# Kernel optimization log

Hardware: AMD Instinct MI355X
Metric: run time of the kernel (lower is better)

The kernel has to match this reference:

```python
import jax, jax.numpy as jnp
import numpy as np

N, E = 50000, 800000
H, KC, EC, NH = 64, 64, 32, 4   # hidden, key, edge channels, heads
HPH, KPH = H // NH, KC // NH    # per-head value/key dims (16, 16)


def ssp(x):
    # ShiftedSoftplus
    return jax.nn.softplus(x) - jnp.log(2.0).astype(x.dtype)


def grouped_lin(x, w):
    # x: (N, NH, in_per_head), w: (NH, out_per_head, in_per_head)
    # equivalent to Conv1d(kernel=1, groups=NH, bias=False)
    return jnp.einsum('nhi,hoi->nho', x, w)


def lin(x, w, b):
    return x @ w.T + b


def segment_softmax(logits, seg, num_segments):
    # logits: (E, NH), seg: (E,)
    m = jax.ops.segment_max(logits, seg, num_segments=num_segments)
    m = jnp.where(jnp.isfinite(m), m, 0.0)
    e = jnp.exp(logits - m[seg])
    s = jax.ops.segment_sum(e, seg, num_segments=num_segments)
    return e / s[seg]


def setup_inputs() -> dict:
    key = jax.random.key(0)
    ks = jax.random.split(key, 24)
    sc = 0.05
    inp = {
        'x': jax.random.normal(ks[0], (N, H), jnp.float32),
        'edge_index': jax.random.randint(ks[1], (2, E), 0, N, jnp.int64),
        'edge_attr': jax.random.normal(ks[2], (E, EC), jnp.float32),
        # grouped 1x1 convs (block-diagonal linears), no bias
        'k_w': jax.random.normal(ks[3], (NH, KPH, HPH), jnp.float32) * sc,
        'q_w': jax.random.normal(ks[4], (NH, KPH, HPH), jnp.float32) * sc,
        'v_w': jax.random.normal(ks[5], (NH, HPH, HPH), jnp.float32) * sc,
        # weight_k_net: Linear(EC,KPH) -> ssp -> Linear(KPH,KPH)
        'wkn_w1': jax.random.normal(ks[6], (KPH, EC), jnp.float32) * sc,
        'wkn_b1': jnp.zeros((KPH,), jnp.float32),
        'wkn_w2': jax.random.normal(ks[7], (KPH, KPH), jnp.float32) * sc,
        'wkn_b2': jnp.zeros((KPH,), jnp.float32),
        'wkl_w': jax.random.normal(ks[8], (KPH, KPH), jnp.float32) * sc,
        'wkl_b': jnp.zeros((KPH,), jnp.float32),
        # weight_v_net: Linear(EC,HPH) -> ssp -> Linear(HPH,HPH)
        'wvn_w1': jax.random.normal(ks[9], (HPH, EC), jnp.float32) * sc,
        'wvn_b1': jnp.zeros((HPH,), jnp.float32),
        'wvn_w2': jax.random.normal(ks[10], (HPH, HPH), jnp.float32) * sc,
        'wvn_b2': jnp.zeros((HPH,), jnp.float32),
        'wvl_w': jax.random.normal(ks[11], (HPH, HPH), jnp.float32) * sc,
        'wvl_b': jnp.zeros((HPH,), jnp.float32),
        'cen_w': jax.random.normal(ks[12], (H, H), jnp.float32) * sc,
        'cen_b': jnp.zeros((H,), jnp.float32),
        'out_w': jax.random.normal(ks[13], (H, H), jnp.float32) * sc,
        'out_b': jnp.zeros((H,), jnp.float32),
    }
    return inp


def reference(x, edge_index, edge_attr, k_w, q_w, v_w,
              wkn_w1, wkn_b1, wkn_w2, wkn_b2, wkl_w, wkl_b,
              wvn_w1, wvn_b1, wvn_w2, wvn_b2, wvl_w, wvl_b,
              cen_w, cen_b, out_w, out_b):
    n = x.shape[0]
    row, col = edge_index[0], edge_index[1]
    xh = x.reshape(n, NH, HPH)                       # per-head split of channels
    h_keys = grouped_lin(xh, k_w)                    # (N, NH, KPH)
    h_queries = grouped_lin(xh, q_w)                 # (N, NH, KPH)
    h_values = grouped_lin(xh, v_w)                  # (N, NH, HPH)

    W_k = lin(ssp(lin(edge_attr, wkn_w1, wkn_b1)), wkn_w2, wkn_b2)   # (E, KPH)
    keys_j = lin(W_k[:, None, :] * h_keys[col], wkl_w, wkl_b)        # (E, NH, KPH)
    queries_i = h_queries[row]                                       # (E, NH, KPH)
    qk_ij = jnp.sum(queries_i * keys_j, axis=-1)                     # (E, NH)
    alpha = segment_softmax(qk_ij, row, n)                           # (E, NH)

    W_v = lin(ssp(lin(edge_attr, wvn_w1, wvn_b1)), wvn_w2, wvn_b2)   # (E, HPH)
    msg_j = lin(W_v[:, None, :] * h_values[col], wvl_w, wvl_b)       # (E, NH, HPH)
    msg_j = alpha[:, :, None] * msg_j
    aggr = jax.ops.segment_sum(msg_j, row, num_segments=n).reshape(n, H)

    out = lin(x, cen_w, cen_b) + aggr
    return lin(ssp(out), out_w, out_b)
```

## Files before the change

### kernel.cpp

```cpp
#include <hip/hip_runtime.h>
#include <math.h>
#include <stdint.h>

#define NN 50000
#define NE 800000
#define HD 64
#define ECH 32
#define NHEAD 4
#define NBLK 196
#define NEBLK (NE / 256)

static_assert(NE % 256 == 0, "edge kernel assumes full blocks");

typedef __attribute__((ext_vector_type(8))) short bf8;
typedef __attribute__((ext_vector_type(4))) float f32x4;
typedef __attribute__((ext_vector_type(2))) float v2f;
typedef __attribute__((ext_vector_type(2))) __bf16 v2bf;

#define LOG2E 1.44269504088896340736f
#define LN2   0.69314718055994530942f

__device__ __forceinline__ float ssp_f(float v) {
    float t = __builtin_amdgcn_exp2f(-fabsf(v) * LOG2E);
    return fmaxf(v, 0.0f) + LN2 * __builtin_amdgcn_logf(1.0f + t) - LN2;
}
__device__ __forceinline__ float bf2f(uint32_t b) { return __uint_as_float(b << 16); }

__device__ __forceinline__ uint32_t cvt_pk_bf16(float lo, float hi) {
    v2f v = {lo, hi};
    v2bf b = __builtin_convertvector(v, v2bf);
    return __builtin_bit_cast(uint32_t, b);
}
__device__ __forceinline__ v2f bfpair(uint32_t p) {
    v2f r;
    r.x = __uint_as_float(p << 16);
    r.y = __uint_as_float(p & 0xffff0000u);
    return r;
}
__device__ __forceinline__ uint4 pack8c(const float* s) {
    uint4 r;
    r.x = cvt_pk_bf16(s[0], s[1]);
    r.y = cvt_pk_bf16(s[2], s[3]);
    r.z = cvt_pk_bf16(s[4], s[5]);
    r.w = cvt_pk_bf16(s[6], s[7]);
    return r;
}
__device__ __forceinline__ bf8 pack_bf8(float4 a, float4 b) {
    union { uint32_t u[4]; bf8 v; } r;
    r.u[0] = cvt_pk_bf16(a.x, a.y);
    r.u[1] = cvt_pk_bf16(a.z, a.w);
    r.u[2] = cvt_pk_bf16(b.x, b.y);
    r.u[3] = cvt_pk_bf16(b.z, b.w);
    return r.v;
}
__device__ __forceinline__ bf8 zero_bf8() {
    bf8 r;
    #pragma unroll
    for (int i = 0; i < 8; ++i) r[i] = 0;
    return r;
}

__global__ __launch_bounds__(256) void node_count_kernel(
    const float* __restrict__ x, const int* __restrict__ ei,
    const float* __restrict__ k_w, const float* __restrict__ q_w, const float* __restrict__ v_w,
    const float* __restrict__ wkl_w, const float* __restrict__ wkl_b,
    uint16_t* __restrict__ qtq, uint16_t* __restrict__ hkv,
    int* __restrict__ counts)
{
    atomicAdd(counts + ei[blockIdx.x * 256 + threadIdx.x], 1);

    if (blockIdx.x >= NBLK) return;
    __shared__ float skw[NHEAD * 256], sqw[NHEAD * 256], svw[NHEAD * 256];
    __shared__ float s_kl[256], s_klb[16];
    for (int i = threadIdx.x; i < NHEAD * 256; i += 256) {
        skw[i] = k_w[i]; sqw[i] = q_w[i]; svw[i] = v_w[i];
    }
    if (threadIdx.x < 256) s_kl[threadIdx.x] = wkl_w[threadIdx.x] * LOG2E;
    if (threadIdx.x < 16) s_klb[threadIdx.x] = wkl_b[threadIdx.x] * LOG2E;
    __syncthreads();
    int n = blockIdx.x * 256 + threadIdx.x;
    if (n >= NN) return;
    const float* xn = x + (size_t)n * HD;
    uint16_t* qrow = qtq + (size_t)n * 72;
    uint16_t* kvrow = hkv + (size_t)n * 128;
    float qbv[NHEAD];
    for (int h = 0; h < NHEAD; ++h) {
        v2f xr2[8];
        {
            const float4* xp = (const float4*)(xn + h * 16);
            #pragma unroll
            for (int j = 0; j < 4; ++j) {
                float4 t4 = xp[j];
                xr2[2 * j] = (v2f){t4.x, t4.y};
                xr2[2 * j + 1] = (v2f){t4.z, t4.w};
            }
        }
        float rq[16], rk[16], rv[16];
        for (int o = 0; o < 16; ++o) {
            const v2f* wq = (const v2f*)(sqw + h * 256 + o * 16);
            const v2f* wk = (const v2f*)(skw + h * 256 + o * 16);
            const v2f* wv = (const v2f*)(svw + h * 256 + o * 16);
            v2f sq = {0.f, 0.f}, sk = {0.f, 0.f}, sv = {0.f, 0.f};
            #pragma unroll
            for (int j = 0; j < 8; ++j) {
                sq += xr2[j] * wq[j];
                sk += xr2[j] * wk[j];
                sv += xr2[j] * wv[j];
            }
            rq[o] = sq.x + sq.y; rk[o] = sk.x + sk.y; rv[o] = sv.x + sv.y;
        }
        float rqt[16];
        #pragma unroll
        for (int ip = 0; ip < 8; ++ip) {
            v2f s2 = {0.f, 0.f};
            #pragma unroll
            for (int o = 0; o < 16; ++o) {
                v2f kl = *(const v2f*)(s_kl + o * 16 + 2 * ip);
                v2f q2 = {rq[o], rq[o]};
                s2 += q2 * kl;
            }
            rqt[2 * ip] = s2.x; rqt[2 * ip + 1] = s2.y;
        }
        float qbh = 0.f;
        #pragma unroll
        for (int o = 0; o < 16; ++o) qbh += rq[o] * s_klb[o];
        qbv[h] = qbh;

        uint4* oq = (uint4*)(qrow + h * 16);
        uint4* ok = (uint4*)(kvrow + h * 16);
        uint4* ov = (uint4*)(kvrow + 64 + h * 16);
        oq[0] = pack8c(rqt); oq[1] = pack8c(rqt + 8);
        ok[0] = pack8c(rk);  ok[1] = pack8c(rk + 8);
        ov[0] = pack8c(rv);  ov[1] = pack8c(rv + 8);
    }
    *(float4*)(qrow + 64) = *(float4*)&qbv[0];
}

__global__ __launch_bounds__(256) void scan_bsum_kernel(
    const int* __restrict__ counts, int* __restrict__ bsum)
{
    __shared__ int sd[256];
    int i = blockIdx.x * 256 + threadIdx.x;
    sd[threadIdx.x] = (i < NN) ? counts[i] : 0;
    __syncthreads();
    for (int s = 128; s > 0; s >>= 1) {
        if (threadIdx.x < (unsigned)s) sd[threadIdx.x] += sd[threadIdx.x + s];
        __syncthreads();
    }
    if (threadIdx.x == 0) bsum[blockIdx.x] = sd[0];
}

__global__ __launch_bounds__(256) void scan_top_kernel(int* __restrict__ bsum)
{
    __shared__ int tmp[256];
    int v = (threadIdx.x < NBLK) ? bsum[threadIdx.x] : 0;
    tmp[threadIdx.x] = v;
    __syncthreads();
    for (int d = 1; d < 256; d <<= 1) {
        int t = (threadIdx.x >= (unsigned)d) ? tmp[threadIdx.x - d] : 0;
        __syncthreads();
        tmp[threadIdx.x] += t;
        __syncthreads();
    }
    if (threadIdx.x < NBLK) bsum[threadIdx.x] = tmp[threadIdx.x] - v;
}

__global__ __launch_bounds__(256) void scan_final_kernel(
    const int* __restrict__ counts, const int* __restrict__ bsum,
    int* __restrict__ offsets, int* __restrict__ cursor)
{
    __shared__ int tmp[256];
    int i = blockIdx.x * 256 + threadIdx.x;
    int v = (i < NN) ? counts[i] : 0;
    tmp[threadIdx.x] = v;
    __syncthreads();
    for (int d = 1; d < 256; d <<= 1) {
        int t = (threadIdx.x >= (unsigned)d) ? tmp[threadIdx.x - d] : 0;
        __syncthreads();
        tmp[threadIdx.x] += t;
        __syncthreads();
    }
    int excl = tmp[threadIdx.x] - v + bsum[blockIdx.x];
    if (i < NN) { offsets[i] = excl; cursor[i] = excl; }
}

__global__ __launch_bounds__(256) void scatter_kernel(
    const int* __restrict__ ei, int* __restrict__ cursor,
    int* __restrict__ elist, uint32_t* __restrict__ rcp)
{
    int e = blockIdx.x * 256 + threadIdx.x;
    if (e >= NE) return;
    int r = ei[e];
    int c = ei[NE + e];
    int pos = atomicAdd(cursor + r, 1);
    elist[pos] = e;
    rcp[pos] = ((uint32_t)r << 16) | (uint32_t)c;
}

__global__ __launch_bounds__(256) void edge_compute_kernel(
    const int* __restrict__ elist, const uint32_t* __restrict__ rcp,
    const float* __restrict__ ea,
    const float* __restrict__ wkn_w1, const float* __restrict__ wkn_b1,
    const float* __restrict__ wkn_w2, const float* __restrict__ wkn_b2,
    const float* __restrict__ wvn_w1, const float* __restrict__ wvn_b1,
    const float* __restrict__ wvn_w2, const float* __restrict__ wvn_b2,
    const uint16_t* __restrict__ qtq, const uint16_t* __restrict__ hkv,
    uint16_t* __restrict__ payload, float* __restrict__ wfac)
{
    __shared__ uint16_t s_trA[4][64][24];
    __shared__ uint16_t s_trB[4][64][24];

    const int w = threadIdx.x >> 6;
    const int L = threadIdx.x & 63;
    const int m = L & 15;
    const int g = L >> 4;
    const int ebase = blockIdx.x * 256 + w * 64;

    int eidv[4];
    uint32_t rcv[4];
    #pragma unroll
    for (int t = 0; t < 4; ++t) eidv[t] = elist[ebase + 16 * t + m];
    #pragma unroll
    for (int t = 0; t < 4; ++t) rcv[t] = rcp[ebase + 16 * t + m];

    bf8 eaf[4];
    #pragma unroll
    for (int t = 0; t < 4; ++t) {
        const float* er = ea + (size_t)eidv[t] * ECH + 8 * g;
        eaf[t] = pack_bf8(*(const float4*)er, *(const float4*)(er + 4));
    }
    bf8 w1kf, w1vf, w2kf, w2vf;
    {
        const float* p = wkn_w1 + m * 32 + 8 * g;
        w1kf = pack_bf8(*(const float4*)p, *(const float4*)(p + 4));
        p = wvn_w1 + m * 32 + 8 * g;
        w1vf = pack_bf8(*(const float4*)p, *(const float4*)(p + 4));
        if (g < 2) {
            p = wkn_w2 + m * 16 + 8 * g;
            w2kf = pack_bf8(*(const float4*)p, *(const float4*)(p + 4));
            p = wvn_w2 + m * 16 + 8 * g;
            w2vf = pack_bf8(*(const float4*)p, *(const float4*)(p + 4));
        } else {
            w2kf = zero_bf8(); w2vf = zero_bf8();
        }
    }
    float4 b1k = *(const float4*)(wkn_b1 + 4 * g);
    float4 b1v = *(const float4*)(wvn_b1 + 4 * g);
    float4 b2k = *(const float4*)(wkn_b2 + 4 * g);
    float4 b2v = *(const float4*)(wvn_b2 + 4 * g);

    #pragma unroll
    for (int t = 0; t < 4; ++t) {
        f32x4 acc = {b1k.x, b1k.y, b1k.z, b1k.w};
        acc = __builtin_amdgcn_mfma_f32_16x16x32_bf16(w1kf, eaf[t], acc, 0, 0, 0);
        uint2 pk;
        pk.x = cvt_pk_bf16(ssp_f(acc[0]), ssp_f(acc[1]));
        pk.y = cvt_pk_bf16(ssp_f(acc[2]), ssp_f(acc[3]));
        *(uint2*)&s_trA[w][16 * t + m][4 * g] = pk;
    }
    bf8 l1k[4];
    #pragma unroll
    for (int t = 0; t < 4; ++t)
        l1k[t] = (g < 2) ? *(const bf8*)&s_trA[w][16 * t + m][8 * g] : zero_bf8();
    #pragma unroll
    for (int t = 0; t < 4; ++t) {
        f32x4 acc = {b1v.x, b1v.y, b1v.z, b1v.w};
        acc = __builtin_amdgcn_mfma_f32_16x16x32_bf16(w1vf, eaf[t], acc, 0, 0, 0);
        uint2 pk;
        pk.x = cvt_pk_bf16(ssp_f(acc[0]), ssp_f(acc[1]));
        pk.y = cvt_pk_bf16(ssp_f(acc[2]), ssp_f(acc[3]));
        *(uint2*)&s_trA[w][16 * t + m][4 * g] = pk;
    }
    bf8 l1v[4];
    #pragma unroll
    for (int t = 0; t < 4; ++t)
        l1v[t] = (g < 2) ? *(const bf8*)&s_trA[w][16 * t + m][8 * g] : zero_bf8();

    #pragma unroll
    for (int t = 0; t < 4; ++t) {
        f32x4 acc = {b2k.x, b2k.y, b2k.z, b2k.w};
        acc = __builtin_amdgcn_mfma_f32_16x16x32_bf16(w2kf, l1k[t], acc, 0, 0, 0);
        uint2 pk;
        pk.x = cvt_pk_bf16(acc[0], acc[1]);
        pk.y = cvt_pk_bf16(acc[2], acc[3]);
        *(uint2*)&s_trB[w][16 * t + m][4 * g] = pk;

        f32x4 accv = {b2v.x, b2v.y, b2v.z, b2v.w};
        accv = __builtin_amdgcn_mfma_f32_16x16x32_bf16(w2vf, l1v[t], accv, 0, 0, 0);
        uint2 pv;
        pv.x = cvt_pk_bf16(accv[0], accv[1]);
        pv.y = cvt_pk_bf16(accv[2], accv[3]);
        *(uint2*)&s_trA[w][16 * t + m][4 * g] = pv;
    }

    #pragma unroll
    for (int t = 0; t < 4; ++t) {
        const int E = ebase + 16 * t + m;
        const int row = (int)(rcv[t] >> 16), col = (int)(rcv[t] & 0xffffu);

        uint32_t wk_u[8], wv_u[8];
        *(uint4*)&wk_u[0] = *(const uint4*)&s_trB[w][16 * t + m][0];
        *(uint4*)&wk_u[4] = *(const uint4*)&s_trB[w][16 * t + m][8];
        *(uint4*)&wv_u[0] = *(const uint4*)&s_trA[w][16 * t + m][0];
        *(uint4*)&wv_u[4] = *(const uint4*)&s_trA[w][16 * t + m][8];

        const uint16_t* qrow = qtq + (size_t)row * 72;
        const uint16_t* kvrow = hkv + (size_t)col * 128;
        uint32_t q_u[8], k_u[8], v_u[8];
        *(uint4*)&q_u[0] = *(const uint4*)(qrow + 16 * g);
        *(uint4*)&q_u[4] = *(const uint4*)(qrow + 16 * g + 8);
        *(uint4*)&k_u[0] = *(const uint4*)(kvrow + 16 * g);
        *(uint4*)&k_u[4] = *(const uint4*)(kvrow + 16 * g + 8);
        *(uint4*)&v_u[0] = *(const uint4*)(kvrow + 64 + 16 * g);
        *(uint4*)&v_u[4] = *(const uint4*)(kvrow + 64 + 16 * g + 8);

        v2f qk2 = {0.f, 0.f};
        #pragma unroll
        for (int i = 0; i < 8; ++i)
            qk2 += bfpair(q_u[i]) * (bfpair(wk_u[i]) * bfpair(k_u[i]));
        float qk = *(const float*)(qrow + 64 + 2 * g) + qk2.x + qk2.y;
        float wgt = __builtin_amdgcn_exp2f(qk);
        v2f wgt2 = {wgt, wgt};

        uint32_t po[8];
        #pragma unroll
        for (int i = 0; i < 8; ++i) {
            v2f o2 = (bfpair(wv_u[i]) * bfpair(v_u[i])) * wgt2;
            po[i] = cvt_pk_bf16(o2.x, o2.y);
        }
        uint4* pd = (uint4*)(payload + (size_t)E * HD + 16 * g);
        pd[0] = *(uint4*)&po[0];
        pd[1] = *(uint4*)&po[4];
        wfac[(size_t)E * NHEAD + g] = wgt;
    }
}

__global__ __launch_bounds__(256) void gather_kernel(
    const uint16_t* __restrict__ payload, const float* __restrict__ wfac,
    const int* __restrict__ offsets, const int* __restrict__ counts,
    float* __restrict__ mout)
{
    const int n = (blockIdx.x * 256 + threadIdx.x) >> 6;
    if (n >= NN) return;
    const int L = threadIdx.x & 63;
    const int q = L & 7;
    const int g = L >> 3;
    const int h = q >> 1;

    const int st = offsets[n];
    const int deg = counts[n];

    v2f u2[4] = {{0.f,0.f},{0.f,0.f},{0.f,0.f},{0.f,0.f}};
    float ds = 0.f;
    const uint16_t* pp = payload + (size_t)st * HD + 8 * q;
    const float* wp = wfac + (size_t)st * NHEAD + h;
    const int iters = (deg + 7) >> 3;
    for (int i = 0; i < iters; i += 2) {
        const int e0 = 8 * i + g;
        const int e1 = e0 + 8;
        if (e0 < deg) {
            uint4 pv = *(const uint4*)(pp + (size_t)e0 * HD);
            u2[0] += bfpair(pv.x); u2[1] += bfpair(pv.y);
            u2[2] += bfpair(pv.z); u2[3] += bfpair(pv.w);
            ds += wp[(size_t)e0 * NHEAD];
        }
        if (e1 < deg) {
            uint4 pv = *(const uint4*)(pp + (size_t)e1 * HD);
            u2[0] += bfpair(pv.x); u2[1] += bfpair(pv.y);
            u2[2] += bfpair(pv.z); u2[3] += bfpair(pv.w);
            ds += wp[(size_t)e1 * NHEAD];
        }
    }
    #pragma unroll
    for (int s = 8; s < 64; s <<= 1) {
        #pragma unroll
        for (int j = 0; j < 4; ++j) {
            u2[j].x += __shfl_xor(u2[j].x, s);
            u2[j].y += __shfl_xor(u2[j].y, s);
        }
        ds += __shfl_xor(ds, s);
    }
    if (g == 0) {
        float inv = (deg > 0) ? (1.f / ds) : 0.f;
        float r0[4] = {u2[0].x * inv, u2[0].y * inv, u2[1].x * inv, u2[1].y * inv};
        float r1[4] = {u2[2].x * inv, u2[2].y * inv, u2[3].x * inv, u2[3].y * inv};
        float* mr = mout + (size_t)n * HD + 8 * q;
        *(float4*)mr = *(float4*)r0;
        *(float4*)(mr + 4) = *(float4*)r1;
    }
}

__global__ __launch_bounds__(256) void finalize_kernel(
    const float* __restrict__ x, const float* __restrict__ m,
    const int* __restrict__ counts,
    const float* __restrict__ wvl_w, const float* __restrict__ wvl_b,
    const float* __restrict__ cen_w, const float* __restrict__ cen_b,
    const float* __restrict__ out_w, const float* __restrict__ out_b,
    float* __restrict__ out)
{
    __shared__ float s_cw[4096], s_ow[4096];
    __shared__ float s_x[4][64], s_m[4][64], s_t[4][64];
    for (int idx = threadIdx.x; idx < 4096; idx += 256) {
        int o = idx & 63, i = idx >> 6;
        s_cw[i * 64 + o] = cen_w[o * 64 + i];
        s_ow[i * 64 + o] = out_w[o * 64 + i];
    }
    __syncthreads();

    const int l = threadIdx.x >> 6;
    const int c = threadIdx.x & 63;
    const int hh = c >> 4;

    float wvlr[16];
    #pragma unroll
    for (int i = 0; i < 16; ++i) wvlr[i] = wvl_w[(c & 15) * 16 + i];
    const float vlb = wvl_b[c & 15];
    const float cb = cen_b[c];
    const float ob = out_b[c];

    const int n0 = blockIdx.x * 64 + l * 16;
    for (int t = 0; t < 16; ++t) {
        const int n = n0 + t;
        const bool valid = n < NN;
        const int deg = valid ? counts[n] : 0;
        s_x[l][c] = valid ? x[(size_t)n * HD + c] : 0.f;
        s_m[l][c] = valid ? m[(size_t)n * HD + c] : 0.f;

        float aggr = 0.f;
        if (deg > 0) {
            float s = vlb;
            #pragma unroll
            for (int i = 0; i < 16; ++i) s += s_m[l][hh * 16 + i] * wvlr[i];
            aggr = s;
        }
        float sc = cb;
        #pragma unroll 8
        for (int i = 0; i < 64; ++i) sc += s_x[l][i] * s_cw[i * 64 + c];
        sc += aggr;
        s_t[l][c] = ssp_f(sc);
        float so = ob;
        #pragma unroll 8
        for (int i = 0; i < 64; ++i) so += s_t[l][i] * s_ow[i * 64 + c];
        if (valid) out[(size_t)n * HD + c] = so;
    }
}

extern "C" void kernel_launch(void* const* d_in, const int* in_sizes, int n_in,
                              void* d_out, int out_size, void* d_ws, size_t ws_size,
                              hipStream_t stream)
{
    const float* x      = (const float*)d_in[0];
    const int*   ei     = (const int*)d_in[1];
    const float* ea     = (const float*)d_in[2];
    const float* k_w    = (const float*)d_in[3];
    const float* q_w    = (const float*)d_in[4];
    const float* v_w    = (const float*)d_in[5];
    const float* wkn_w1 = (const float*)d_in[6];
    const float* wkn_b1 = (const float*)d_in[7];
    const float* wkn_w2 = (const float*)d_in[8];
    const float* wkn_b2 = (const float*)d_in[9];
    const float* wkl_w  = (const float*)d_in[10];
    const float* wkl_b  = (const float*)d_in[11];
    const float* wvn_w1 = (const float*)d_in[12];
    const float* wvn_b1 = (const float*)d_in[13];
    const float* wvn_w2 = (const float*)d_in[14];
    const float* wvn_b2 = (const float*)d_in[15];
    const float* wvl_w  = (const float*)d_in[16];
    const float* wvl_b  = (const float*)d_in[17];
    const float* cen_w  = (const float*)d_in[18];
    const float* cen_b  = (const float*)d_in[19];
    const float* out_w  = (const float*)d_in[20];
    const float* out_b  = (const float*)d_in[21];
    float* out = (float*)d_out;

    float* wfac  = (float*)d_ws;
    uint16_t* qtq = (uint16_t*)(wfac + (size_t)NE * NHEAD);
    uint16_t* hkv = qtq + (size_t)NN * 72;
    uint16_t* payload = hkv + (size_t)NN * 128;
    uint32_t* rcp = (uint32_t*)(payload + (size_t)NE * HD);
    int* elist   = (int*)(rcp + (size_t)NE);
    int* counts  = elist + NE;
    int* bsum    = counts + NN;
    int* offsets = bsum + 256;
    int* cursor  = offsets + NN;
    float* mbuf  = (float*)hkv;

    hipMemsetAsync(counts, 0, (size_t)NN * sizeof(int), stream);
    node_count_kernel<<<NEBLK, 256, 0, stream>>>(
        x, ei, k_w, q_w, v_w, wkl_w, wkl_b, qtq, hkv, counts);
    scan_bsum_kernel<<<NBLK, 256, 0, stream>>>(counts, bsum);
    scan_top_kernel<<<1, 256, 0, stream>>>(bsum);
    scan_final_kernel<<<NBLK, 256, 0, stream>>>(counts, bsum, offsets, cursor);
    scatter_kernel<<<NEBLK, 256, 0, stream>>>(ei, cursor, elist, rcp);
    edge_compute_kernel<<<NEBLK, 256, 0, stream>>>(
        elist, rcp, ea, wkn_w1, wkn_b1, wkn_w2, wkn_b2,
        wvn_w1, wvn_b1, wvn_w2, wvn_b2,
        qtq, hkv, payload, wfac);
    gather_kernel<<<(NN * 64) / 256, 256, 0, stream>>>(
        payload, wfac, offsets, counts, mbuf);
    finalize_kernel<<<(NN + 63) / 64, 256, 0, stream>>>(
        x, mbuf, counts, wvl_w, wvl_b, cen_w, cen_b, out_w, out_b, out);
}
```

Baseline: 450.1 us.

## Fuse gather into edge kernel via in-wave segmented scan and atomics

Removes the per-edge bf16 payload and weight buffers and the separate gather kernel. Each wave now runs a segmented inclusive scan over 16 row-sorted edges using shuffles, and the segment ends atomically add fp32 partial sums and softmax denominators into per-node buffers. The finalize kernel divides by the accumulated denominator. This avoids writing and re-reading about 100MB of payload. In exchange it adds shuffle work, many float atomics to global memory, and an extra memset, and summation order becomes nondeterministic.

Result: slower. 789.3 us (+75.4%).

```diff
diff --git a/kernel.cpp b/kernel.cpp
--- a/kernel.cpp
+++ b/kernel.cpp
@@ -205,7 +205,7 @@
     const float* __restrict__ wvn_w1, const float* __restrict__ wvn_b1,
     const float* __restrict__ wvn_w2, const float* __restrict__ wvn_b2,
     const uint16_t* __restrict__ qtq, const uint16_t* __restrict__ hkv,
-    uint16_t* __restrict__ payload, float* __restrict__ wfac)
+    float* __restrict__ mraw, float* __restrict__ dsb)
 {
     __shared__ uint16_t s_trA[4][64][24];
     __shared__ uint16_t s_trB[4][64][24];
@@ -295,7 +295,6 @@
 
     #pragma unroll
     for (int t = 0; t < 4; ++t) {
-        const int E = ebase + 16 * t + m;
         const int row = (int)(rcv[t] >> 16), col = (int)(rcv[t] & 0xffffu);
 
         uint32_t wk_u[8], wv_u[8];
@@ -322,77 +321,39 @@
         float wgt = __builtin_amdgcn_exp2f(qk);
         v2f wgt2 = {wgt, wgt};
 
-        uint32_t po[8];
+        float o[17];
         #pragma unroll
         for (int i = 0; i < 8; ++i) {
             v2f o2 = (bfpair(wv_u[i]) * bfpair(v_u[i])) * wgt2;
-            po[i] = cvt_pk_bf16(o2.x, o2.y);
-        }
-        uint4* pd = (uint4*)(payload + (size_t)E * HD + 16 * g);
-        pd[0] = *(uint4*)&po[0];
-        pd[1] = *(uint4*)&po[4];
-        wfac[(size_t)E * NHEAD + g] = wgt;
-    }
-}
-
-__global__ __launch_bounds__(256) void gather_kernel(
-    const uint16_t* __restrict__ payload, const float* __restrict__ wfac,
-    const int* __restrict__ offsets, const int* __restrict__ counts,
-    float* __restrict__ mout)
-{
-    const int n = (blockIdx.x * 256 + threadIdx.x) >> 6;
-    if (n >= NN) return;
-    const int L = threadIdx.x & 63;
-    const int q = L & 7;
-    const int g = L >> 3;
-    const int h = q >> 1;
-
-    const int st = offsets[n];
-    const int deg = counts[n];
-
-    v2f u2[4] = {{0.f,0.f},{0.f,0.f},{0.f,0.f},{0.f,0.f}};
-    float ds = 0.f;
-    const uint16_t* pp = payload + (size_t)st * HD + 8 * q;
-    const float* wp = wfac + (size_t)st * NHEAD + h;
-    const int iters = (deg + 7) >> 3;
-    for (int i = 0; i < iters; i += 2) {
-        const int e0 = 8 * i + g;
-        const int e1 = e0 + 8;
-        if (e0 < deg) {
-            uint4 pv = *(const uint4*)(pp + (size_t)e0 * HD);
-            u2[0] += bfpair(pv.x); u2[1] += bfpair(pv.y);
-            u2[2] += bfpair(pv.z); u2[3] += bfpair(pv.w);
-            ds += wp[(size_t)e0 * NHEAD];
-        }
-        if (e1 < deg) {
-            uint4 pv = *(const uint4*)(pp + (size_t)e1 * HD);
-            u2[0] += bfpair(pv.x); u2[1] += bfpair(pv.y);
-            u2[2] += bfpair(pv.z); u2[3] += bfpair(pv.w);
-            ds += wp[(size_t)e1 * NHEAD];
-        }
-    }
-    #pragma unroll
-    for (int s = 8; s < 64; s <<= 1) {
+            o[2 * i] = o2.x; o[2 * i + 1] = o2.y;
+        }
+        o[16] = wgt;
+
         #pragma unroll
-        for (int j = 0; j < 4; ++j) {
-            u2[j].x += __shfl_xor(u2[j].x, s);
-            u2[j].y += __shfl_xor(u2[j].y, s);
-        }
-        ds += __shfl_xor(ds, s);
-    }
-    if (g == 0) {
-        float inv = (deg > 0) ? (1.f / ds) : 0.f;
-        float r0[4] = {u2[0].x * inv, u2[0].y * inv, u2[1].x * inv, u2[1].y * inv};
-        float r1[4] = {u2[2].x * inv, u2[2].y * inv, u2[3].x * inv, u2[3].y * inv};
-        float* mr = mout + (size_t)n * HD + 8 * q;
-        *(float4*)mr = *(float4*)r0;
-        *(float4*)(mr + 4) = *(float4*)r1;
+        for (int d = 1; d < 16; d <<= 1) {
+            const int srcl = (L - d) & 63;
+            const int prow = __shfl(row, srcl);
+            const bool take = (m >= d) && (prow == row);
+            #pragma unroll
+            for (int i = 0; i < 17; ++i) {
+                float pv = __shfl(o[i], srcl);
+                o[i] += take ? pv : 0.0f;
+            }
+        }
+        const int nrow = __shfl(row, (L + 1) & 63);
+        const bool segend = (m == 15) || (nrow != row);
+        if (segend) {
+            float* mr = mraw + (size_t)row * HD + 16 * g;
+            #pragma unroll
+            for (int i = 0; i < 16; ++i) atomicAdd(mr + i, o[i]);
+            atomicAdd(dsb + (size_t)row * NHEAD + g, o[16]);
+        }
     }
 }
 
 __global__ __launch_bounds__(256) void finalize_kernel(
-    const float* __restrict__ x, const float* __restrict__ m,
-    const int* __restrict__ counts,
+    const float* __restrict__ x, const float* __restrict__ mraw,
+    const float* __restrict__ dsb, const int* __restrict__ counts,
     const float* __restrict__ wvl_w, const float* __restrict__ wvl_b,
     const float* __restrict__ cen_w, const float* __restrict__ cen_b,
     const float* __restrict__ out_w, const float* __restrict__ out_b,
@@ -424,7 +385,12 @@
         const bool valid = n < NN;
         const int deg = valid ? counts[n] : 0;
         s_x[l][c] = valid ? x[(size_t)n * HD + c] : 0.f;
-        s_m[l][c] = valid ? m[(size_t)n * HD + c] : 0.f;
+        float mv = 0.f;
+        if (deg > 0) {
+            float dsv = dsb[(size_t)n * NHEAD + hh];
+            mv = mraw[(size_t)n * HD + c] * (1.0f / dsv);
+        }
+        s_m[l][c] = mv;
 
         float aggr = 0.f;
         if (deg > 0) {
@@ -473,19 +439,19 @@
     const float* out_b  = (const float*)d_in[21];
     float* out = (float*)d_out;
 
-    float* wfac  = (float*)d_ws;
-    uint16_t* qtq = (uint16_t*)(wfac + (size_t)NE * NHEAD);
+    uint16_t* qtq = (uint16_t*)d_ws;
     uint16_t* hkv = qtq + (size_t)NN * 72;
-    uint16_t* payload = hkv + (size_t)NN * 128;
-    uint32_t* rcp = (uint32_t*)(payload + (size_t)NE * HD);
+    float* mraw  = (float*)(hkv + (size_t)NN * 128);
+    float* dsb   = mraw + (size_t)NN * HD;
+    uint32_t* rcp = (uint32_t*)(dsb + (size_t)NN * NHEAD);
     int* elist   = (int*)(rcp + (size_t)NE);
     int* counts  = elist + NE;
     int* bsum    = counts + NN;
     int* offsets = bsum + 256;
     int* cursor  = offsets + NN;
-    float* mbuf  = (float*)hkv;
 
     hipMemsetAsync(counts, 0, (size_t)NN * sizeof(int), stream);
+    hipMemsetAsync(mraw, 0, (size_t)NN * (HD + NHEAD) * sizeof(float), stream);
     node_count_kernel<<<NEBLK, 256, 0, stream>>>(
         x, ei, k_w, q_w, v_w, wkl_w, wkl_b, qtq, hkv, counts);
     scan_bsum_kernel<<<NBLK, 256, 0, stream>>>(counts, bsum);
@@ -495,9 +461,7 @@
     edge_compute_kernel<<<NEBLK, 256, 0, stream>>>(
         elist, rcp, ea, wkn_w1, wkn_b1, wkn_w2, wkn_b2,
         wvn_w1, wvn_b1, wvn_w2, wvn_b2,
-        qtq, hkv, payload, wfac);
-    gather_kernel<<<(NN * 64) / 256, 256, 0, stream>>>(
-        payload, wfac, offsets, counts, mbuf);
+        qtq, hkv, mraw, dsb);
     finalize_kernel<<<(NN + 63) / 64, 256, 0, stream>>>(
-        x, mbuf, counts, wvl_w, wvl_b, cen_w, cen_b, out_w, out_b, out);
-}
+        x, mraw, dsb, counts, wvl_w, wvl_b, cen_w, cen_b, out_w, out_b, out);
+}
```

## Record per-edge rank during counting and drop separate scatter kernel

Applied to the files above, without the earlier changes.

The counting atomic now returns each edge's rank within its destination row, and the edge kernel computes its CSR slot as offsets[row]+rank. This removes the scatter pass and the elist/rcp buffers. The edge kernel now reads edge_attr and edge_index in their original contiguous order and scatters its payload writes instead of gathering edge_attr reads. In exchange, rows and columns are read as full ints rather than a packed word, and the edge kernel does an extra indirect offsets lookup.

Measured after the change: 448.6 us. No clear change (-0.3%).

```diff
diff --git a/kernel.cpp b/kernel.cpp
--- a/kernel.cpp
+++ b/kernel.cpp
@@ -65,9 +65,13 @@
     const float* __restrict__ k_w, const float* __restrict__ q_w, const float* __restrict__ v_w,
     const float* __restrict__ wkl_w, const float* __restrict__ wkl_b,
     uint16_t* __restrict__ qtq, uint16_t* __restrict__ hkv,
-    int* __restrict__ counts)
-{
-    atomicAdd(counts + ei[blockIdx.x * 256 + threadIdx.x], 1);
+    int* __restrict__ counts, int* __restrict__ rank)
+{
+    {
+        int e = blockIdx.x * 256 + threadIdx.x;
+        int r = ei[e];
+        rank[e] = atomicAdd(counts + r, 1);
+    }
 
     if (blockIdx.x >= NBLK) return;
     __shared__ float skw[NHEAD * 256], sqw[NHEAD * 256], svw[NHEAD * 256];
@@ -167,7 +171,7 @@
 
 __global__ __launch_bounds__(256) void scan_final_kernel(
     const int* __restrict__ counts, const int* __restrict__ bsum,
-    int* __restrict__ offsets, int* __restrict__ cursor)
+    int* __restrict__ offsets)
 {
     __shared__ int tmp[256];
     int i = blockIdx.x * 256 + threadIdx.x;
@@ -181,24 +185,12 @@
         __syncthreads();
     }
     int excl = tmp[threadIdx.x] - v + bsum[blockIdx.x];
-    if (i < NN) { offsets[i] = excl; cursor[i] = excl; }
-}
-
-__global__ __launch_bounds__(256) void scatter_kernel(
-    const int* __restrict__ ei, int* __restrict__ cursor,
-    int* __restrict__ elist, uint32_t* __restrict__ rcp)
-{
-    int e = blockIdx.x * 256 + threadIdx.x;
-    if (e >= NE) return;
-    int r = ei[e];
-    int c = ei[NE + e];
-    int pos = atomicAdd(cursor + r, 1);
-    elist[pos] = e;
-    rcp[pos] = ((uint32_t)r << 16) | (uint32_t)c;
+    if (i < NN) offsets[i] = excl;
 }
 
 __global__ __launch_bounds__(256) void edge_compute_kernel(
-    const int* __restrict__ elist, const uint32_t* __restrict__ rcp,
+    const int* __restrict__ ei, const int* __restrict__ rank,
+    const int* __restrict__ offsets,
     const float* __restrict__ ea,
     const float* __restrict__ wkn_w1, const float* __restrict__ wkn_b1,
     const float* __restrict__ wkn_w2, const float* __restrict__ wkn_b2,
@@ -216,17 +208,23 @@
     const int g = L >> 4;
     const int ebase = blockIdx.x * 256 + w * 64;
 
-    int eidv[4];
-    uint32_t rcv[4];
-    #pragma unroll
-    for (int t = 0; t < 4; ++t) eidv[t] = elist[ebase + 16 * t + m];
-    #pragma unroll
-    for (int t = 0; t < 4; ++t) rcv[t] = rcp[ebase + 16 * t + m];
+    int rows[4], cols[4], posv[4];
+    #pragma unroll
+    for (int t = 0; t < 4; ++t) {
+        const int e = ebase + 16 * t + m;
+        rows[t] = ei[e];
+        cols[t] = ei[NE + e];
+    }
+    #pragma unroll
+    for (int t = 0; t < 4; ++t) {
+        const int e = ebase + 16 * t + m;
+        posv[t] = offsets[rows[t]] + rank[e];
+    }
 
     bf8 eaf[4];
     #pragma unroll
     for (int t = 0; t < 4; ++t) {
-        const float* er = ea + (size_t)eidv[t] * ECH + 8 * g;
+        const float* er = ea + (size_t)(ebase + 16 * t + m) * ECH + 8 * g;
         eaf[t] = pack_bf8(*(const float4*)er, *(const float4*)(er + 4));
     }
     bf8 w1kf, w1vf, w2kf, w2vf;
@@ -295,8 +293,7 @@
 
     #pragma unroll
     for (int t = 0; t < 4; ++t) {
-        const int E = ebase + 16 * t + m;
-        const int row = (int)(rcv[t] >> 16), col = (int)(rcv[t] & 0xffffu);
+        const int row = rows[t], col = cols[t];
 
         uint32_t wk_u[8], wv_u[8];
         *(uint4*)&wk_u[0] = *(const uint4*)&s_trB[w][16 * t + m][0];
@@ -328,10 +325,10 @@
             v2f o2 = (bfpair(wv_u[i]) * bfpair(v_u[i])) * wgt2;
             po[i] = cvt_pk_bf16(o2.x, o2.y);
         }
-        uint4* pd = (uint4*)(payload + (size_t)E * HD + 16 * g);
+        uint4* pd = (uint4*)(payload + (size_t)posv[t] * HD + 16 * g);
         pd[0] = *(uint4*)&po[0];
         pd[1] = *(uint4*)&po[4];
-        wfac[(size_t)E * NHEAD + g] = wgt;
+        wfac[(size_t)posv[t] * NHEAD + g] = wgt;
     }
 }
 
@@ -477,23 +474,20 @@
     uint16_t* qtq = (uint16_t*)(wfac + (size_t)NE * NHEAD);
     uint16_t* hkv = qtq + (size_t)NN * 72;
     uint16_t* payload = hkv + (size_t)NN * 128;
-    uint32_t* rcp = (uint32_t*)(payload + (size_t)NE * HD);
-    int* elist   = (int*)(rcp + (size_t)NE);
-    int* counts  = elist + NE;
+    int* rank    = (int*)(payload + (size_t)NE * HD);
+    int* counts  = rank + NE;
     int* bsum    = counts + NN;
     int* offsets = bsum + 256;
-    int* cursor  = offsets + NN;
     float* mbuf  = (float*)hkv;
 
     hipMemsetAsync(counts, 0, (size_t)NN * sizeof(int), stream);
     node_count_kernel<<<NEBLK, 256, 0, stream>>>(
-        x, ei, k_w, q_w, v_w, wkl_w, wkl_b, qtq, hkv, counts);
+        x, ei, k_w, q_w, v_w, wkl_w, wkl_b, qtq, hkv, counts, rank);
     scan_bsum_kernel<<<NBLK, 256, 0, stream>>>(counts, bsum);
     scan_top_kernel<<<1, 256, 0, stream>>>(bsum);
-    scan_final_kernel<<<NBLK, 256, 0, stream>>>(counts, bsum, offsets, cursor);
-    scatter_kernel<<<NEBLK, 256, 0, stream>>>(ei, cursor, elist, rcp);
+    scan_final_kernel<<<NBLK, 256, 0, stream>>>(counts, bsum, offsets);
     edge_compute_kernel<<<NEBLK, 256, 0, stream>>>(
-        elist, rcp, ea, wkn_w1, wkn_b1, wkn_w2, wkn_b2,
+        ei, rank, offsets, ea, wkn_w1, wkn_b1, wkn_w2, wkn_b2,
         wvn_w1, wvn_b1, wvn_w2, wvn_b2,
         qtq, hkv, payload, wfac);
     gather_kernel<<<(NN * 64) / 256, 256, 0, stream>>>(
```
